# Optimization experiments

Hardware: AMD Instinct MI355X
Metric: run time of the kernel (lower is better)

The kernel has to match this reference:

```python
import jax, jax.numpy as jnp
import numpy as np

N = 200_000       # nodes
K = 16            # fixed in-degree
E = N * K         # edges
G = 4_000         # graphs (50 nodes each)
F_IN, H1, H2, OUT = 25, 16, 8, 2
EPS = 1e-5        # PyG std aggregator epsilon


def setup_inputs() -> dict:
    key = jax.random.key(0)
    ks = jax.random.split(key, 10)
    x = jax.random.normal(ks[0], (N, F_IN), jnp.float32)
    src = jax.random.randint(ks[1], (E,), 0, N)
    dst = jnp.repeat(jnp.arange(N), K)          # every node gets K incoming edges
    edge_index = jnp.stack([src, dst]).astype(jnp.int32)
    batch = jnp.repeat(jnp.arange(G), N // G).astype(jnp.int32)

    def lin(k, o, i):
        s = 1.0 / np.sqrt(i)
        kw, kb = jax.random.split(k)
        return (jax.random.uniform(kw, (o, i), jnp.float32, -s, s),
                jax.random.uniform(kb, (o,), jnp.float32, -s, s))

    w1_pre, b1_pre = lin(ks[2], F_IN, 2 * F_IN)
    w1_post, b1_post = lin(ks[3], H1, 12 * F_IN)
    w1_lin, b1_lin = lin(ks[4], H1, H1)
    w2_pre, b2_pre = lin(ks[5], H1, 2 * H1)
    w2_post, b2_post = lin(ks[6], H2, 12 * H1)
    w2_lin, b2_lin = lin(ks[7], H2, H2)
    fc_w, fc_b = lin(ks[8], OUT, H2)
    return dict(x=x, edge_index=edge_index, batch=batch,
                w1_pre=w1_pre, b1_pre=b1_pre, w1_post=w1_post, b1_post=b1_post,
                w1_lin=w1_lin, b1_lin=b1_lin,
                w2_pre=w2_pre, b2_pre=b2_pre, w2_post=w2_post, b2_post=b2_post,
                w2_lin=w2_lin, b2_lin=b2_lin, fc_w=fc_w, fc_b=fc_b)


def pna_conv(x, edge_index, wp, bp, wo, bo, wl, bl):
    src, dst = edge_index[0], edge_index[1]
    # message: pre-MLP on concat([x_i, x_j])  (x_i = target, x_j = source)
    m = jnp.concatenate([x[dst], x[src]], axis=-1) @ wp.T + bp  # [E, F]
    cnt = jax.ops.segment_sum(jnp.ones((m.shape[0],), m.dtype), dst, N)  # in-degree
    cnt_c = jnp.maximum(cnt, 1.0)[:, None]
    mean = jax.ops.segment_sum(m, dst, N) / cnt_c
    mean2 = jax.ops.segment_sum(m * m, dst, N) / cnt_c
    std = jnp.sqrt(jax.nn.relu(mean2 - mean * mean) + EPS)
    has = cnt[:, None] > 0
    mn = jnp.where(has, jax.ops.segment_min(m, dst, N), 0.0)
    mx = jnp.where(has, jax.ops.segment_max(m, dst, N), 0.0)
    agg = jnp.concatenate([mean, mn, mx, std], axis=-1)  # [N, 4F]
    # degree scalers (identity / amplification / attenuation)
    logd = jnp.log(jnp.maximum(cnt, 1.0) + 1.0)[:, None]
    avg_log = jnp.mean(jnp.log(cnt + 1.0))
    out = jnp.concatenate([agg, agg * (logd / avg_log), agg * (avg_log / logd)], axis=-1)
    out = out @ wo.T + bo   # post MLP
    return out @ wl.T + bl  # final lin


def reference(x, edge_index, batch,
              w1_pre, b1_pre, w1_post, b1_post, w1_lin, b1_lin,
              w2_pre, b2_pre, w2_post, b2_post, w2_lin, b2_lin,
              fc_w, fc_b):
    h = jax.nn.relu(pna_conv(x, edge_index, w1_pre, b1_pre, w1_post, b1_post, w1_lin, b1_lin))
    # dropout is identity in eval mode
    h = jax.nn.relu(pna_conv(h, edge_index, w2_pre, b2_pre, w2_post, b2_post, w2_lin, b2_lin))
    pooled = jax.ops.segment_sum(h, batch, G)  # global_add_pool -> [G, H2]
    logits = pooled @ fc_w.T + fc_b
    return jax.nn.log_softmax(logits, axis=1)
```

## Files before the change

kernel.cpp:

```cpp
#include <hip/hip_runtime.h>
#include <math.h>

#define N_NODES 200000
#define K_DEG 16
#define G_GRAPHS 4000
#define F_IN 25
#define EPSV 1e-5f

__device__ inline unsigned short f2bf(float f) {
    unsigned int u = __float_as_uint(f);
    u += 0x7fff + ((u >> 16) & 1);
    return (unsigned short)(u >> 16);
}
__device__ inline float bf2f(unsigned short h) {
    return __uint_as_float(((unsigned int)h) << 16);
}

__global__ void prep(const float* __restrict__ w1_pre, const float* __restrict__ b1_pre,
                     const float* __restrict__ w1_post, const float* __restrict__ b1_post,
                     const float* __restrict__ w1_lin, const float* __restrict__ b1_lin,
                     const float* __restrict__ w2_pre, const float* __restrict__ b2_pre,
                     const float* __restrict__ w2_post, const float* __restrict__ b2_post,
                     const float* __restrict__ w2_lin, const float* __restrict__ b2_lin,
                     float* __restrict__ C1, float* __restrict__ bvp1, float* __restrict__ P1,
                     float* __restrict__ C2, float* __restrict__ bvp2, float* __restrict__ P2) {
    int tid = threadIdx.x;
    if (blockIdx.x == 0) {
        __shared__ float wp[16 * 300];
        __shared__ float wl[256];
        __shared__ float m1[1600];
        __shared__ float a1[400];
        for (int i = tid; i < 4800; i += 256) wp[i] = w1_post[i];
        for (int i = tid; i < 256; i += 256) wl[i] = w1_lin[i];
        __syncthreads();
        for (int i = tid; i < 1600; i += 256) {
            int o = i / 100, j = i % 100;
            float s = 0.f;
            for (int h = 0; h < 16; ++h)
                s += wl[o * 16 + h] * (wp[h * 300 + j] + wp[h * 300 + 100 + j] + wp[h * 300 + 200 + j]);
            m1[i] = s;
            C1[i] = s;
        }
        __syncthreads();
        for (int i = tid; i < 400; i += 256) {
            int o = i / 25, f = i % 25;
            a1[i] = m1[o * 100 + f] + m1[o * 100 + 25 + f] + m1[o * 100 + 50 + f];
        }
        __syncthreads();
        for (int i = tid; i < 400; i += 256) {
            int o = i / 25, k = i % 25;
            float s = 0.f;
            for (int f = 0; f < 25; ++f) s += a1[o * 25 + f] * w1_pre[f * 50 + k];
            P1[i] = s;
        }
        if (tid < 16) {
            float s = b1_lin[tid];
            for (int h = 0; h < 16; ++h) s += wl[tid * 16 + h] * b1_post[h];
            for (int f = 0; f < 25; ++f) s += a1[tid * 25 + f] * b1_pre[f];
            bvp1[tid] = s;
        }
    } else {
        __shared__ float wp[8 * 192];
        __shared__ float wl[64];
        __shared__ float m2[512];
        __shared__ float a2[128];
        for (int i = tid; i < 1536; i += 256) wp[i] = w2_post[i];
        if (tid < 64) wl[tid] = w2_lin[tid];
        __syncthreads();
        for (int i = tid; i < 512; i += 256) {
            int o = i / 64, j = i % 64;
            float s = 0.f;
            for (int h = 0; h < 8; ++h)
                s += wl[o * 8 + h] * (wp[h * 192 + j] + wp[h * 192 + 64 + j] + wp[h * 192 + 128 + j]);
            m2[i] = s;
            C2[i] = s;
        }
        __syncthreads();
        if (tid < 128) {
            int o = tid / 16, f = tid % 16;
            a2[tid] = m2[o * 64 + f] + m2[o * 64 + 16 + f] + m2[o * 64 + 32 + f];
        }
        __syncthreads();
        if (tid < 128) {
            int o = tid / 16, k = tid % 16;
            float s = 0.f;
            for (int f = 0; f < 16; ++f) s += a2[o * 16 + f] * w2_pre[f * 32 + k];
            P2[tid] = s;
        }
        if (tid < 8) {
            float s = b2_lin[tid];
            for (int h = 0; h < 8; ++h) s += wl[tid * 8 + h] * b2_post[h];
            for (int f = 0; f < 16; ++f) s += a2[tid * 16 + f] * b2_pre[f];
            bvp2[tid] = s;
        }
    }
}

__global__ void __launch_bounds__(256) pre1(const float* __restrict__ x,
                                            const float* __restrict__ w1_pre,
                                            const float* __restrict__ P1,
                                            unsigned int* __restrict__ c1b_dw,
                                            float* __restrict__ d1) {
    __shared__ float xs[256 * 25];
    __shared__ float wls[25 * 25];
    __shared__ float pls[16 * 25];
    __shared__ unsigned int otile[256 * 17];
    int tid = threadIdx.x;
    int base = blockIdx.x * 256;
    for (int i = tid; i < 6400; i += 256) {
        int g = base * 25 + i;
        xs[i] = (g < N_NODES * F_IN) ? x[g] : 0.f;
    }
    for (int i = tid; i < 625; i += 256) {
        int f = i / 25, k = i % 25;
        wls[i] = w1_pre[f * 50 + 25 + k];
    }
    for (int i = tid; i < 400; i += 256) pls[i] = P1[i];
    __syncthreads();

    float xr[25];
#pragma unroll
    for (int k = 0; k < 25; ++k) xr[k] = xs[tid * 25 + k];

    unsigned int pk[16];
#pragma unroll
    for (int j = 0; j < 16; ++j) pk[j] = 0;
#pragma unroll
    for (int f = 0; f < 25; ++f) {
        float s = 0.f;
#pragma unroll
        for (int k = 0; k < 25; ++k) s += wls[f * 25 + k] * xr[k];
        unsigned int b = f2bf(s);
        pk[f >> 1] |= (f & 1) ? (b << 16) : b;
    }
#pragma unroll
    for (int j = 0; j < 16; ++j) otile[tid * 17 + j] = pk[j];
    __syncthreads();
    for (int i = tid; i < 4096; i += 256) {
        int g = base * 16 + i;
        if (g < N_NODES * 16) c1b_dw[g] = otile[(i >> 4) * 17 + (i & 15)];
    }
    __syncthreads();

    float* ftile = (float*)otile;
#pragma unroll
    for (int o = 0; o < 16; ++o) {
        float s = 0.f;
#pragma unroll
        for (int k = 0; k < 25; ++k) s += pls[o * 25 + k] * xr[k];
        ftile[tid * 17 + o] = s;
    }
    __syncthreads();
    for (int i = tid; i < 4096; i += 256) {
        int g = base * 16 + i;
        if (g < N_NODES * 16) d1[g] = ftile[(i >> 4) * 17 + (i & 15)];
    }
}

#define A1_NPB 8
__global__ void __launch_bounds__(256) agg1(const unsigned short* __restrict__ c1b,
                                            const int* __restrict__ src,
                                            const float* __restrict__ d1,
                                            const float* __restrict__ C1,
                                            const float* __restrict__ bvp1,
                                            const float* __restrict__ w2_pre,
                                            const float* __restrict__ P2,
                                            unsigned short* __restrict__ c2b,
                                            float* __restrict__ d2) {
    __shared__ float cs[16 * 100];
    __shared__ float aggs[A1_NPB * 100];
    __shared__ float h1s[A1_NPB * 17];
    __shared__ float ws2[16 * 17];
    __shared__ float p2s[8 * 17];
    __shared__ float bvs[16];
    int tid = threadIdx.x;
    for (int i = tid; i < 1600; i += 256) cs[i] = C1[i];
    if (tid < 256) {
        int f = tid >> 4, k = tid & 15;
        ws2[f * 17 + k] = w2_pre[f * 32 + 16 + k];
    }
    if (tid < 128) {
        int o = tid >> 4, k = tid & 15;
        p2s[o * 17 + k] = P2[tid];
    }
    if (tid < 16) bvs[tid] = bvp1[tid];
    __syncthreads();

    int group = tid >> 5;
    int lane  = tid & 31;
    int n = blockIdx.x * A1_NPB + group;
    if (lane < F_IN) {
        const int* sp = src + n * K_DEG;
        int idx[K_DEG];
#pragma unroll
        for (int e = 0; e < K_DEG; ++e) idx[e] = sp[e];
        float v[K_DEG];
#pragma unroll
        for (int e = 0; e < K_DEG; ++e) v[e] = bf2f(c1b[idx[e] * 32 + lane]);
        float s = 0.f, sq = 0.f, mn = 1e30f, mx = -1e30f;
#pragma unroll
        for (int e = 0; e < K_DEG; ++e) {
            float m = v[e];
            s += m; sq += m * m; mn = fminf(mn, m); mx = fmaxf(mx, m);
        }
        float mean = s * (1.f / 16.f);
        float var  = sq * (1.f / 16.f) - mean * mean;
        float sd   = sqrtf(fmaxf(var, 0.f) + EPSV);
        aggs[group * 100 + lane]      = mean;
        aggs[group * 100 + 25 + lane] = mn;
        aggs[group * 100 + 50 + lane] = mx;
        aggs[group * 100 + 75 + lane] = sd;
    }
    __syncthreads();

    if (tid < A1_NPB * 16) {
        int nl = tid >> 4, o = tid & 15;
        int nn = blockIdx.x * A1_NPB + nl;
        float s = bvs[o] + d1[nn * 16 + o];
        const float4* c4 = (const float4*)(cs + o * 100);
        const float4* a4 = (const float4*)(aggs + nl * 100);
#pragma unroll
        for (int j = 0; j < 25; ++j) {
            float4 cv = c4[j], av = a4[j];
            s += cv.x * av.x + cv.y * av.y + cv.z * av.z + cv.w * av.w;
        }
        h1s[nl * 17 + o] = fmaxf(s, 0.f);
    }
    __syncthreads();

    if (tid < A1_NPB * 16) {
        int nl = tid >> 4, f = tid & 15;
        int nn = blockIdx.x * A1_NPB + nl;
        const float* hr = h1s + nl * 17;
        float s = 0.f;
#pragma unroll
        for (int k = 0; k < 16; ++k) s += ws2[f * 17 + k] * hr[k];
        c2b[nn * 16 + f] = f2bf(s);
    } else if (tid < A1_NPB * 16 + A1_NPB * 8) {
        int t = tid - A1_NPB * 16;
        int nl = t >> 3, o = t & 7;
        int nn = blockIdx.x * A1_NPB + nl;
        const float* hr = h1s + nl * 17;
        float s = 0.f;
#pragma unroll
        for (int k = 0; k < 16; ++k) s += p2s[o * 17 + k] * hr[k];
        d2[nn * 8 + o] = s;
    }
}

#define A2_NPB 16
__global__ void __launch_bounds__(256) agg2(const unsigned short* __restrict__ c2b,
                                            const int* __restrict__ src,
                                            const float* __restrict__ d2,
                                            const float* __restrict__ C2,
                                            const float* __restrict__ bvp2,
                                            float* __restrict__ h2) {
    __shared__ float cs[8 * 68];
    __shared__ float ag[A2_NPB * 68];
    __shared__ float bvs[8];
    int tid = threadIdx.x;
    for (int i = tid; i < 512; i += 256) cs[(i >> 6) * 68 + (i & 63)] = C2[i];
    if (tid < 8) bvs[tid] = bvp2[tid];
    __syncthreads();

    int group = tid >> 4;
    int lane  = tid & 15;
    int n = blockIdx.x * A2_NPB + group;
    {
        const int* sp = src + n * K_DEG;
        int idx[K_DEG];
#pragma unroll
        for (int e = 0; e < K_DEG; ++e) idx[e] = sp[e];
        float v[K_DEG];
#pragma unroll
        for (int e = 0; e < K_DEG; ++e) v[e] = bf2f(c2b[idx[e] * 16 + lane]);
        float s = 0.f, sq = 0.f, mn = 1e30f, mx = -1e30f;
#pragma unroll
        for (int e = 0; e < K_DEG; ++e) {
            float m = v[e];
            s += m; sq += m * m; mn = fminf(mn, m); mx = fmaxf(mx, m);
        }
        float mean = s * (1.f / 16.f);
        float var  = sq * (1.f / 16.f) - mean * mean;
        float sd   = sqrtf(fmaxf(var, 0.f) + EPSV);
        ag[group * 68 + lane]      = mean;
        ag[group * 68 + 16 + lane] = mn;
        ag[group * 68 + 32 + lane] = mx;
        ag[group * 68 + 48 + lane] = sd;
    }
    __syncthreads();

    if (tid < A2_NPB * 8) {
        int nl = tid >> 3, o = tid & 7;
        int nn = blockIdx.x * A2_NPB + nl;
        float s = bvs[o] + d2[nn * 8 + o];
        const float4* c4 = (const float4*)(cs + o * 68);
        const float4* a4 = (const float4*)(ag + nl * 68);
#pragma unroll
        for (int j = 0; j < 16; ++j) {
            float4 cv = c4[j], av = a4[j];
            s += cv.x * av.x + cv.y * av.y + cv.z * av.z + cv.w * av.w;
        }
        h2[nn * 8 + o] = fmaxf(s, 0.f);
    }
}

__global__ void pool_fc(const float* __restrict__ h2, const float* __restrict__ fc_w,
                        const float* __restrict__ fc_b, float* __restrict__ out) {
    int wave = threadIdx.x >> 6;
    int lane = threadIdx.x & 63;
    int g = blockIdx.x * 4 + wave;
    float s0 = 0.f, s1 = 0.f;
    if (lane < 50) {
        const float* hr = h2 + (g * 50 + lane) * 8;
        float v[8];
#pragma unroll
        for (int o = 0; o < 8; ++o) v[o] = hr[o];
#pragma unroll
        for (int o = 0; o < 8; ++o) { s0 += fc_w[o] * v[o]; s1 += fc_w[8 + o] * v[o]; }
    }
#pragma unroll
    for (int off = 32; off > 0; off >>= 1) {
        s0 += __shfl_down(s0, off);
        s1 += __shfl_down(s1, off);
    }
    if (lane == 0) {
        float l0 = s0 + fc_b[0], l1 = s1 + fc_b[1];
        float m = fmaxf(l0, l1);
        float lse = m + logf(expf(l0 - m) + expf(l1 - m));
        out[g * 2]     = l0 - lse;
        out[g * 2 + 1] = l1 - lse;
    }
}

extern "C" void kernel_launch(void* const* d_in, const int* in_sizes, int n_in,
                              void* d_out, int out_size, void* d_ws, size_t ws_size,
                              hipStream_t stream) {
    const float* x       = (const float*)d_in[0];
    const int*   eidx    = (const int*)d_in[1];
    const float* w1_pre  = (const float*)d_in[3];
    const float* b1_pre  = (const float*)d_in[4];
    const float* w1_post = (const float*)d_in[5];
    const float* b1_post = (const float*)d_in[6];
    const float* w1_lin  = (const float*)d_in[7];
    const float* b1_lin  = (const float*)d_in[8];
    const float* w2_pre  = (const float*)d_in[9];
    const float* b2_pre  = (const float*)d_in[10];
    const float* w2_post = (const float*)d_in[11];
    const float* b2_post = (const float*)d_in[12];
    const float* w2_lin  = (const float*)d_in[13];
    const float* b2_lin  = (const float*)d_in[14];
    const float* fc_w    = (const float*)d_in[15];
    const float* fc_b    = (const float*)d_in[16];
    float* out = (float*)d_out;
    const int* src = eidx;

    char* ws = (char*)d_ws;
    unsigned short* c1b = (unsigned short*)ws;
    unsigned short* c2b = (unsigned short*)(ws + 12800000);
    float* d1  = (float*)(ws + 19200000);
    float* d2  = (float*)(ws + 32000000);
    float* h2  = (float*)(ws + 38400000);
    float* C1   = (float*)(ws + 44800000);
    float* bvp1 = C1 + 1600;
    float* P1   = bvp1 + 16;
    float* C2   = P1 + 400;
    float* bvp2 = C2 + 512;
    float* P2   = bvp2 + 8;

    prep<<<2, 256, 0, stream>>>(w1_pre, b1_pre, w1_post, b1_post, w1_lin, b1_lin,
                                w2_pre, b2_pre, w2_post, b2_post, w2_lin, b2_lin,
                                C1, bvp1, P1, C2, bvp2, P2);
    pre1<<<(N_NODES + 255) / 256, 256, 0, stream>>>(x, w1_pre, P1, (unsigned int*)c1b, d1);
    agg1<<<N_NODES / A1_NPB, 256, 0, stream>>>(c1b, src, d1, C1, bvp1, w2_pre, P2, c2b, d2);
    agg2<<<N_NODES / A2_NPB, 256, 0, stream>>>(c2b, src, d2, C2, bvp2, h2);
    pool_fc<<<G_GRAPHS / 4, 256, 0, stream>>>(h2, fc_w, fc_b, out);
}
```

Before: 258.0 us.

## Gather paired bf16 features as 32-bit words and widen aggregation blocks

The aggregation kernels now read two bf16 features per 32-bit gather instead of one 16-bit gather per lane, and they process twice as many nodes per block (16 and 32). The edge source indices are staged cooperatively into shared memory. The layer-1 post-weight matrix is padded to a 26-stride layout so each lane can handle a feature pair, and the prep kernel is merged into a single block. The intent is to halve gather instructions, fill all threads, and coalesce index loads. The cost is extra padding math and a single-block prep that runs serially.

```diff
diff --git a/kernel.cpp b/kernel.cpp
--- a/kernel.cpp
+++ b/kernel.cpp
@@ -22,77 +22,78 @@
                      const float* __restrict__ w2_pre, const float* __restrict__ b2_pre,
                      const float* __restrict__ w2_post, const float* __restrict__ b2_post,
                      const float* __restrict__ w2_lin, const float* __restrict__ b2_lin,
-                     float* __restrict__ C1, float* __restrict__ bvp1, float* __restrict__ P1,
-                     float* __restrict__ C2, float* __restrict__ bvp2, float* __restrict__ P2) {
+                     float* __restrict__ C1ext, float* __restrict__ bvp1, float* __restrict__ P1,
+                     float* __restrict__ C2p, float* __restrict__ bvp2, float* __restrict__ P2) {
+    __shared__ float wp[4800];
+    __shared__ float wl[256];
+    __shared__ float mm[1600];
+    __shared__ float aa[400];
     int tid = threadIdx.x;
-    if (blockIdx.x == 0) {
-        __shared__ float wp[16 * 300];
-        __shared__ float wl[256];
-        __shared__ float m1[1600];
-        __shared__ float a1[400];
-        for (int i = tid; i < 4800; i += 256) wp[i] = w1_post[i];
-        for (int i = tid; i < 256; i += 256) wl[i] = w1_lin[i];
-        __syncthreads();
-        for (int i = tid; i < 1600; i += 256) {
-            int o = i / 100, j = i % 100;
-            float s = 0.f;
-            for (int h = 0; h < 16; ++h)
-                s += wl[o * 16 + h] * (wp[h * 300 + j] + wp[h * 300 + 100 + j] + wp[h * 300 + 200 + j]);
-            m1[i] = s;
-            C1[i] = s;
-        }
-        __syncthreads();
-        for (int i = tid; i < 400; i += 256) {
-            int o = i / 25, f = i % 25;
-            a1[i] = m1[o * 100 + f] + m1[o * 100 + 25 + f] + m1[o * 100 + 50 + f];
-        }
-        __syncthreads();
-        for (int i = tid; i < 400; i += 256) {
-            int o = i / 25, k = i % 25;
-            float s = 0.f;
-            for (int f = 0; f < 25; ++f) s += a1[o * 25 + f] * w1_pre[f * 50 + k];
-            P1[i] = s;
-        }
-        if (tid < 16) {
-            float s = b1_lin[tid];
-            for (int h = 0; h < 16; ++h) s += wl[tid * 16 + h] * b1_post[h];
-            for (int f = 0; f < 25; ++f) s += a1[tid * 25 + f] * b1_pre[f];
-            bvp1[tid] = s;
-        }
-    } else {
-        __shared__ float wp[8 * 192];
-        __shared__ float wl[64];
-        __shared__ float m2[512];
-        __shared__ float a2[128];
-        for (int i = tid; i < 1536; i += 256) wp[i] = w2_post[i];
-        if (tid < 64) wl[tid] = w2_lin[tid];
-        __syncthreads();
-        for (int i = tid; i < 512; i += 256) {
-            int o = i / 64, j = i % 64;
-            float s = 0.f;
-            for (int h = 0; h < 8; ++h)
-                s += wl[o * 8 + h] * (wp[h * 192 + j] + wp[h * 192 + 64 + j] + wp[h * 192 + 128 + j]);
-            m2[i] = s;
-            C2[i] = s;
-        }
-        __syncthreads();
-        if (tid < 128) {
-            int o = tid / 16, f = tid % 16;
-            a2[tid] = m2[o * 64 + f] + m2[o * 64 + 16 + f] + m2[o * 64 + 32 + f];
-        }
-        __syncthreads();
-        if (tid < 128) {
-            int o = tid / 16, k = tid % 16;
-            float s = 0.f;
-            for (int f = 0; f < 16; ++f) s += a2[o * 16 + f] * w2_pre[f * 32 + k];
-            P2[tid] = s;
-        }
-        if (tid < 8) {
-            float s = b2_lin[tid];
-            for (int h = 0; h < 8; ++h) s += wl[tid * 8 + h] * b2_post[h];
-            for (int f = 0; f < 16; ++f) s += a2[tid * 16 + f] * b2_pre[f];
-            bvp2[tid] = s;
-        }
+    for (int i = tid; i < 4800; i += 256) wp[i] = w1_post[i];
+    if (tid < 256) wl[tid] = w1_lin[tid];
+    __syncthreads();
+    for (int i = tid; i < 1600; i += 256) {
+        int o = i / 100, j = i % 100;
+        float s = 0.f;
+        for (int h = 0; h < 16; ++h)
+            s += wl[o * 16 + h] * (wp[h * 300 + j] + wp[h * 300 + 100 + j] + wp[h * 300 + 200 + j]);
+        mm[i] = s;
+    }
+    __syncthreads();
+    for (int i = tid; i < 400; i += 256) {
+        int o = i / 25, f = i % 25;
+        aa[i] = mm[o * 100 + f] + mm[o * 100 + 25 + f] + mm[o * 100 + 50 + f];
+    }
+    __syncthreads();
+    for (int i = tid; i < 1728; i += 256) {
+        int o = i / 108, c = i % 108;
+        int st = c / 26, f = c % 26;
+        C1ext[i] = (c < 104 && f < 25) ? mm[o * 100 + st * 25 + f] : 0.f;
+    }
+    for (int i = tid; i < 400; i += 256) {
+        int o = i / 25, k = i % 25;
+        float s = 0.f;
+        for (int f = 0; f < 25; ++f) s += aa[o * 25 + f] * w1_pre[f * 50 + k];
+        P1[i] = s;
+    }
+    if (tid < 16) {
+        float s = b1_lin[tid];
+        for (int h = 0; h < 16; ++h) s += wl[tid * 16 + h] * b1_post[h];
+        for (int f = 0; f < 25; ++f) s += aa[tid * 25 + f] * b1_pre[f];
+        bvp1[tid] = s;
+    }
+    __syncthreads();
+    for (int i = tid; i < 1536; i += 256) wp[i] = w2_post[i];
+    if (tid < 64) wl[tid] = w2_lin[tid];
+    __syncthreads();
+    for (int i = tid; i < 512; i += 256) {
+        int o = i / 64, j = i % 64;
+        float s = 0.f;
+        for (int h = 0; h < 8; ++h)
+            s += wl[o * 8 + h] * (wp[h * 192 + j] + wp[h * 192 + 64 + j] + wp[h * 192 + 128 + j]);
+        mm[i] = s;
+    }
+    __syncthreads();
+    if (tid < 128) {
+        int o = tid / 16, f = tid % 16;
+        aa[tid] = mm[o * 64 + f] + mm[o * 64 + 16 + f] + mm[o * 64 + 32 + f];
+    }
+    __syncthreads();
+    for (int i = tid; i < 544; i += 256) {
+        int o = i / 68, c = i % 68;
+        C2p[i] = (c < 64) ? mm[o * 64 + c] : 0.f;
+    }
+    if (tid < 128) {
+        int o = tid / 16, k = tid % 16;
+        float s = 0.f;
+        for (int f = 0; f < 16; ++f) s += aa[o * 16 + f] * w2_pre[f * 32 + k];
+        P2[tid] = s;
+    }
+    if (tid < 8) {
+        float s = b2_lin[tid];
+        for (int h = 0; h < 8; ++h) s += wl[tid * 8 + h] * b2_post[h];
+        for (int f = 0; f < 16; ++f) s += aa[tid * 16 + f] * b2_pre[f];
+        bvp2[tid] = s;
     }
 }
 
@@ -157,70 +158,74 @@
     }
 }
 
-#define A1_NPB 8
-__global__ void __launch_bounds__(256) agg1(const unsigned short* __restrict__ c1b,
+__global__ void __launch_bounds__(256) agg1(const unsigned int* __restrict__ c1u,
                                             const int* __restrict__ src,
                                             const float* __restrict__ d1,
-                                            const float* __restrict__ C1,
+                                            const float* __restrict__ C1ext,
                                             const float* __restrict__ bvp1,
                                             const float* __restrict__ w2_pre,
                                             const float* __restrict__ P2,
                                             unsigned short* __restrict__ c2b,
                                             float* __restrict__ d2) {
-    __shared__ float cs[16 * 100];
-    __shared__ float aggs[A1_NPB * 100];
-    __shared__ float h1s[A1_NPB * 17];
+    __shared__ float cs[16 * 108];
+    __shared__ float aggs[16 * 108];
+    __shared__ float h1s[16 * 17];
     __shared__ float ws2[16 * 17];
     __shared__ float p2s[8 * 17];
     __shared__ float bvs[16];
+    __shared__ int idxs[256];
     int tid = threadIdx.x;
-    for (int i = tid; i < 1600; i += 256) cs[i] = C1[i];
-    if (tid < 256) {
+    for (int i = tid; i < 1728; i += 256) cs[i] = C1ext[i];
+    {
         int f = tid >> 4, k = tid & 15;
         ws2[f * 17 + k] = w2_pre[f * 32 + 16 + k];
     }
-    if (tid < 128) {
-        int o = tid >> 4, k = tid & 15;
-        p2s[o * 17 + k] = P2[tid];
-    }
+    if (tid < 128) p2s[(tid >> 4) * 17 + (tid & 15)] = P2[tid];
     if (tid < 16) bvs[tid] = bvp1[tid];
-    __syncthreads();
-
-    int group = tid >> 5;
-    int lane  = tid & 31;
-    int n = blockIdx.x * A1_NPB + group;
-    if (lane < F_IN) {
-        const int* sp = src + n * K_DEG;
-        int idx[K_DEG];
-#pragma unroll
-        for (int e = 0; e < K_DEG; ++e) idx[e] = sp[e];
-        float v[K_DEG];
-#pragma unroll
-        for (int e = 0; e < K_DEG; ++e) v[e] = bf2f(c1b[idx[e] * 32 + lane]);
-        float s = 0.f, sq = 0.f, mn = 1e30f, mx = -1e30f;
+    idxs[tid] = src[blockIdx.x * 256 + tid];
+    __syncthreads();
+
+    int g = tid >> 4;
+    int L = tid & 15;
+    {
+        int id[K_DEG];
+#pragma unroll
+        for (int e = 0; e < K_DEG; ++e) id[e] = idxs[g * 16 + e];
+        unsigned int v[K_DEG];
+#pragma unroll
+        for (int e = 0; e < K_DEG; ++e) v[e] = c1u[id[e] * 16 + L];
+        float s0 = 0.f, q0 = 0.f, n0 = 1e30f, x0 = -1e30f;
+        float s1 = 0.f, q1 = 0.f, n1 = 1e30f, x1 = -1e30f;
 #pragma unroll
         for (int e = 0; e < K_DEG; ++e) {
-            float m = v[e];
-            s += m; sq += m * m; mn = fminf(mn, m); mx = fmaxf(mx, m);
-        }
-        float mean = s * (1.f / 16.f);
-        float var  = sq * (1.f / 16.f) - mean * mean;
-        float sd   = sqrtf(fmaxf(var, 0.f) + EPSV);
-        aggs[group * 100 + lane]      = mean;
-        aggs[group * 100 + 25 + lane] = mn;
-        aggs[group * 100 + 50 + lane] = mx;
-        aggs[group * 100 + 75 + lane] = sd;
-    }
-    __syncthreads();
-
-    if (tid < A1_NPB * 16) {
+            float a = bf2f((unsigned short)(v[e] & 0xffff));
+            float b = bf2f((unsigned short)(v[e] >> 16));
+            s0 += a; q0 += a * a; n0 = fminf(n0, a); x0 = fmaxf(x0, a);
+            s1 += b; q1 += b * b; n1 = fminf(n1, b); x1 = fmaxf(x1, b);
+        }
+        float me0 = s0 * (1.f / 16.f), me1 = s1 * (1.f / 16.f);
+        float sd0 = sqrtf(fmaxf(q0 * (1.f / 16.f) - me0 * me0, 0.f) + EPSV);
+        float sd1 = sqrtf(fmaxf(q1 * (1.f / 16.f) - me1 * me1, 0.f) + EPSV);
+        if (L < 13) {
+            float* r = aggs + g * 108 + 2 * L;
+            *(float2*)(r)      = make_float2(me0, me1);
+            *(float2*)(r + 26) = make_float2(n0, n1);
+            *(float2*)(r + 52) = make_float2(x0, x1);
+            *(float2*)(r + 78) = make_float2(sd0, sd1);
+        } else if (L == 13) {
+            *(float4*)(aggs + g * 108 + 104) = make_float4(0.f, 0.f, 0.f, 0.f);
+        }
+    }
+    __syncthreads();
+
+    {
         int nl = tid >> 4, o = tid & 15;
-        int nn = blockIdx.x * A1_NPB + nl;
+        int nn = blockIdx.x * 16 + nl;
         float s = bvs[o] + d1[nn * 16 + o];
-        const float4* c4 = (const float4*)(cs + o * 100);
-        const float4* a4 = (const float4*)(aggs + nl * 100);
-#pragma unroll
-        for (int j = 0; j < 25; ++j) {
+        const float4* c4 = (const float4*)(cs + o * 108);
+        const float4* a4 = (const float4*)(aggs + nl * 108);
+#pragma unroll
+        for (int j = 0; j < 27; ++j) {
             float4 cv = c4[j], av = a4[j];
             s += cv.x * av.x + cv.y * av.y + cv.z * av.z + cv.w * av.w;
         }
@@ -228,18 +233,18 @@
     }
     __syncthreads();
 
-    if (tid < A1_NPB * 16) {
+    {
         int nl = tid >> 4, f = tid & 15;
-        int nn = blockIdx.x * A1_NPB + nl;
+        int nn = blockIdx.x * 16 + nl;
         const float* hr = h1s + nl * 17;
         float s = 0.f;
 #pragma unroll
         for (int k = 0; k < 16; ++k) s += ws2[f * 17 + k] * hr[k];
         c2b[nn * 16 + f] = f2bf(s);
-    } else if (tid < A1_NPB * 16 + A1_NPB * 8) {
-        int t = tid - A1_NPB * 16;
-        int nl = t >> 3, o = t & 7;
-        int nn = blockIdx.x * A1_NPB + nl;
+    }
+    if (tid < 128) {
+        int nl = tid >> 3, o = tid & 7;
+        int nn = blockIdx.x * 16 + nl;
         const float* hr = h1s + nl * 17;
         float s = 0.f;
 #pragma unroll
@@ -248,56 +253,61 @@
     }
 }
 
-#define A2_NPB 16
-__global__ void __launch_bounds__(256) agg2(const unsigned short* __restrict__ c2b,
+__global__ void __launch_bounds__(256) agg2(const unsigned int* __restrict__ c2u,
                                             const int* __restrict__ src,
                                             const float* __restrict__ d2,
-                                            const float* __restrict__ C2,
+                                            const float* __restrict__ C2p,
                                             const float* __restrict__ bvp2,
                                             float* __restrict__ h2) {
     __shared__ float cs[8 * 68];
-    __shared__ float ag[A2_NPB * 68];
+    __shared__ float ag[32 * 68];
     __shared__ float bvs[8];
+    __shared__ int idxs[512];
     int tid = threadIdx.x;
-    for (int i = tid; i < 512; i += 256) cs[(i >> 6) * 68 + (i & 63)] = C2[i];
+    for (int i = tid; i < 544; i += 256) cs[i] = C2p[i];
     if (tid < 8) bvs[tid] = bvp2[tid];
-    __syncthreads();
-
-    int group = tid >> 4;
-    int lane  = tid & 15;
-    int n = blockIdx.x * A2_NPB + group;
-    {
-        const int* sp = src + n * K_DEG;
-        int idx[K_DEG];
-#pragma unroll
-        for (int e = 0; e < K_DEG; ++e) idx[e] = sp[e];
-        float v[K_DEG];
-#pragma unroll
-        for (int e = 0; e < K_DEG; ++e) v[e] = bf2f(c2b[idx[e] * 16 + lane]);
-        float s = 0.f, sq = 0.f, mn = 1e30f, mx = -1e30f;
+    idxs[tid] = src[blockIdx.x * 512 + tid];
+    idxs[tid + 256] = src[blockIdx.x * 512 + 256 + tid];
+    __syncthreads();
+
+    int g = tid >> 3;
+    int L = tid & 7;
+    {
+        int id[K_DEG];
+#pragma unroll
+        for (int e = 0; e < K_DEG; ++e) id[e] = idxs[g * 16 + e];
+        unsigned int v[K_DEG];
+#pragma unroll
+        for (int e = 0; e < K_DEG; ++e) v[e] = c2u[id[e] * 8 + L];
+        float s0 = 0.f, q0 = 0.f, n0 = 1e30f, x0 = -1e30f;
+        float s1 = 0.f, q1 = 0.f, n1 = 1e30f, x1 = -1e30f;
 #pragma unroll
         for (int e = 0; e < K_DEG; ++e) {
-            float m = v[e];
-            s += m; sq += m * m; mn = fminf(mn, m); mx = fmaxf(mx, m);
-        }
-        float mean = s * (1.f / 16.f);
-        float var  = sq * (1.f / 16.f) - mean * mean;
-        float sd   = sqrtf(fmaxf(var, 0.f) + EPSV);
-        ag[group * 68 + lane]      = mean;
-        ag[group * 68 + 16 + lane] = mn;
-        ag[group * 68 + 32 + lane] = mx;
-        ag[group * 68 + 48 + lane] = sd;
-    }
-    __syncthreads();
-
-    if (tid < A2_NPB * 8) {
+            float a = bf2f((unsigned short)(v[e] & 0xffff));
+            float b = bf2f((unsigned short)(v[e] >> 16));
+            s0 += a; q0 += a * a; n0 = fminf(n0, a); x0 = fmaxf(x0, a);
+            s1 += b; q1 += b * b; n1 = fminf(n1, b); x1 = fmaxf(x1, b);
+        }
+        float me0 = s0 * (1.f / 16.f), me1 = s1 * (1.f / 16.f);
+        float sd0 = sqrtf(fmaxf(q0 * (1.f / 16.f) - me0 * me0, 0.f) + EPSV);
+        float sd1 = sqrtf(fmaxf(q1 * (1.f / 16.f) - me1 * me1, 0.f) + EPSV);
+        float* r = ag + g * 68 + 2 * L;
+        *(float2*)(r)      = make_float2(me0, me1);
+        *(float2*)(r + 16) = make_float2(n0, n1);
+        *(float2*)(r + 32) = make_float2(x0, x1);
+        *(float2*)(r + 48) = make_float2(sd0, sd1);
+        if (L == 0) *(float4*)(ag + g * 68 + 64) = make_float4(0.f, 0.f, 0.f, 0.f);
+    }
+    __syncthreads();
+
+    {
         int nl = tid >> 3, o = tid & 7;
-        int nn = blockIdx.x * A2_NPB + nl;
+        int nn = blockIdx.x * 32 + nl;
         float s = bvs[o] + d2[nn * 8 + o];
         const float4* c4 = (const float4*)(cs + o * 68);
         const float4* a4 = (const float4*)(ag + nl * 68);
 #pragma unroll
-        for (int j = 0; j < 16; ++j) {
+        for (int j = 0; j < 17; ++j) {
             float4 cv = c4[j], av = a4[j];
             s += cv.x * av.x + cv.y * av.y + cv.z * av.z + cv.w * av.w;
         }
@@ -356,23 +366,23 @@
     const int* src = eidx;
 
     char* ws = (char*)d_ws;
-    unsigned short* c1b = (unsigned short*)ws;
+    unsigned int*   c1u = (unsigned int*)ws;
     unsigned short* c2b = (unsigned short*)(ws + 12800000);
     float* d1  = (float*)(ws + 19200000);
     float* d2  = (float*)(ws + 32000000);
     float* h2  = (float*)(ws + 38400000);
-    float* C1   = (float*)(ws + 44800000);
-    float* bvp1 = C1 + 1600;
-    float* P1   = bvp1 + 16;
-    float* C2   = P1 + 400;
-    float* bvp2 = C2 + 512;
-    float* P2   = bvp2 + 8;
-
-    prep<<<2, 256, 0, stream>>>(w1_pre, b1_pre, w1_post, b1_post, w1_lin, b1_lin,
+    float* C1ext = (float*)(ws + 44800000);
+    float* bvp1  = C1ext + 1728;
+    float* P1    = bvp1 + 16;
+    float* C2p   = P1 + 400;
+    float* bvp2  = C2p + 544;
+    float* P2    = bvp2 + 8;
+
+    prep<<<1, 256, 0, stream>>>(w1_pre, b1_pre, w1_post, b1_post, w1_lin, b1_lin,
                                 w2_pre, b2_pre, w2_post, b2_post, w2_lin, b2_lin,
-                                C1, bvp1, P1, C2, bvp2, P2);
-    pre1<<<(N_NODES + 255) / 256, 256, 0, stream>>>(x, w1_pre, P1, (unsigned int*)c1b, d1);
-    agg1<<<N_NODES / A1_NPB, 256, 0, stream>>>(c1b, src, d1, C1, bvp1, w2_pre, P2, c2b, d2);
-    agg2<<<N_NODES / A2_NPB, 256, 0, stream>>>(c2b, src, d2, C2, bvp2, h2);
+                                C1ext, bvp1, P1, C2p, bvp2, P2);
+    pre1<<<(N_NODES + 255) / 256, 256, 0, stream>>>(x, w1_pre, P1, c1u, d1);
+    agg1<<<N_NODES / 16, 256, 0, stream>>>(c1u, src, d1, C1ext, bvp1, w2_pre, P2, c2b, d2);
+    agg2<<<N_NODES / 32, 256, 0, stream>>>((const unsigned int*)c2b, src, d2, C2p, bvp2, h2);
     pool_fc<<<G_GRAPHS / 4, 256, 0, stream>>>(h2, fc_w, fc_b, out);
 }
```

After: 241.9 us. 6.2% less time.
